# Kernel optimization log

Measured on AMD Instinct MI355X. Metric: run time of the kernel, lower is better.

The kernel has to match this reference:

```python
import jax, jax.numpy as jnp
import numpy as np

N, F, H, O = 16384, 64, 128, 512

def setup_inputs() -> dict:
    key = jax.random.key(0)
    ks = jax.random.split(key, 5)
    # PyTorch Linear default init: U(-1/sqrt(fan_in), 1/sqrt(fan_in))
    lim1 = 1.0  # fan_in = 1 for Linear(1, H)
    lim2 = 1.0 / np.sqrt(H)
    x = jax.random.normal(ks[0], (N, F), dtype=jnp.float32)
    W1 = jax.random.uniform(ks[1], (F, H), minval=-lim1, maxval=lim1, dtype=jnp.float32)
    b1 = jax.random.uniform(ks[2], (F, H), minval=-lim1, maxval=lim1, dtype=jnp.float32)
    W2 = jax.random.uniform(ks[3], (F, H, O), minval=-lim2, maxval=lim2, dtype=jnp.float32)
    b2 = jax.random.uniform(ks[4], (F, O), minval=-lim2, maxval=lim2, dtype=jnp.float32)
    return {"x": x, "W1": W1, "b1": b1, "W2": W2, "b2": b2}

def reference(x, W1, b1, W2, b2):
    # Per-feature MLP: h_f = W2_f @ elu(x_f * w1_f + b1_f) + b2_f, summed over f.
    # pre: [N, F, H] = outer-product of each scalar feature with its W1 row
    pre = x[:, :, None] * W1[None, :, :] + b1[None, :, :]
    a = jax.nn.elu(pre)                                  # [N, F, H]
    h = jnp.einsum('nfh,fho->no', a, W2)                 # sum over f and h
    h = h + jnp.sum(b2, axis=0)[None, :]                 # biases summed over F
    return h / jnp.sqrt(jnp.float32(F))
```

## Files before the change

### kernel.cpp

```cpp
#include <hip/hip_runtime.h>
#include <cstdint>

#define NROWS 16384
#define FDIM 64
#define HDIM 128
#define ODIM 512
#define KDIM 8192

#define BM 128
#define BN 256
#define BK 64
#define NSTEPS (KDIM / BK)

typedef short bf16x8 __attribute__((ext_vector_type(8)));
typedef float f32x4 __attribute__((ext_vector_type(4)));
typedef uint32_t u32x4 __attribute__((ext_vector_type(4)));

__device__ __forceinline__ uint16_t rne_bf16(float f) {
  uint32_t u = __builtin_bit_cast(uint32_t, f);
  u += 0x7fffu + ((u >> 16) & 1u);
  return (uint16_t)(u >> 16);
}

__global__ void prep_w2t(const float* __restrict__ W2, uint16_t* __restrict__ W2T) {
  __shared__ float tile[64][65];
  const int k0 = blockIdx.x * 64;
  const int o0 = blockIdx.y * 64;
  const int tx = threadIdx.x;
  const int ty = threadIdx.y;
#pragma unroll
  for (int j = 0; j < 8; ++j)
    tile[ty + 8 * j][tx] = W2[(size_t)(k0 + ty + 8 * j) * ODIM + o0 + tx];
  __syncthreads();
#pragma unroll
  for (int j = 0; j < 8; ++j)
    W2T[(size_t)(o0 + ty + 8 * j) * KDIM + k0 + tx] = rne_bf16(tile[tx][ty + 8 * j]);
}

__global__ void prep_b2sum(const float* __restrict__ b2, float* __restrict__ b2sum) {
  const int t = blockIdx.x * 256 + threadIdx.x;
  float s = 0.f;
#pragma unroll
  for (int f = 0; f < FDIM; ++f) s += b2[(size_t)f * ODIM + t];
  b2sum[t] = s;
}

__global__ __launch_bounds__(512, 2) void mlp_gemm(
    const float* __restrict__ x, const float* __restrict__ W1,
    const float* __restrict__ b1, const uint16_t* __restrict__ W2T,
    const float* __restrict__ b2sum, float* __restrict__ out) {
  __shared__ __align__(16) uint16_t As0[BM * BK];
  __shared__ __align__(16) uint16_t As1[BM * BK];
  __shared__ __align__(16) uint16_t Bs0[BN * BK];
  __shared__ __align__(16) uint16_t Bs1[BN * BK];

  const int tid = threadIdx.x;
  const int bid = blockIdx.x;
  const int g = bid & 7;
  const int o0 = (g >> 2) * BN;
  const int m0 = ((bid >> 3) * 4 + (g & 3)) * BM;

  const int wid = tid >> 6;
  const int lane = tid & 63;
  const int wm = wid >> 2;
  const int wni = wid & 3;
  const int q = lane >> 4;
  const int r = lane & 15;

  const int ar = tid >> 3;
  const int ac = tid & 7;
  const int brow = lane >> 3;
  const int bcg = (lane & 7) ^ brow;

  const float* xp0 = x + (size_t)(m0 + ar) * FDIM;
  const float* xp1 = x + (size_t)(m0 + 64 + ar) * FDIM;
  const int aw0 = ar * BK + ((ac ^ (ar & 7)) * 8);
  const int aw1 = (ar + 64) * BK + ((ac ^ (ar & 7)) * 8);

  f32x4 acc[4][4];
#pragma unroll
  for (int i = 0; i < 4; ++i)
#pragma unroll
    for (int j = 0; j < 4; ++j) acc[i][j] = {0.f, 0.f, 0.f, 0.f};

  auto stage = [&](uint16_t* Ab, uint16_t* Bb, int kk) {
#pragma unroll
    for (int j = 0; j < 4; ++j) {
      const int chunk = wid * 4 + j;
      const uint16_t* gp =
          W2T + (size_t)(o0 + chunk * 8 + brow) * KDIM + kk * BK + bcg * 8;
      uint16_t* lp = Bb + chunk * 512;
      __builtin_amdgcn_global_load_lds(
          (const __attribute__((address_space(1))) uint32_t*)gp,
          (__attribute__((address_space(3))) uint32_t*)lp, 16, 0, 0);
    }
    const int f = kk >> 1;
    const int hoff = (kk & 1) * 64 + ac * 8;
    const float xv0 = xp0[f];
    const float xv1 = xp1[f];
    float w1f[8], b1f[8];
    *(f32x4*)&w1f[0] = *(const f32x4*)(W1 + (size_t)f * HDIM + hoff);
    *(f32x4*)&w1f[4] = *(const f32x4*)(W1 + (size_t)f * HDIM + hoff + 4);
    *(f32x4*)&b1f[0] = *(const f32x4*)(b1 + (size_t)f * HDIM + hoff);
    *(f32x4*)&b1f[4] = *(const f32x4*)(b1 + (size_t)f * HDIM + hoff + 4);
    u32x4 ov0, ov1;
#pragma unroll
    for (int p = 0; p < 4; ++p) {
      float a0 = fmaf(xv0, w1f[2 * p], b1f[2 * p]);
      float a1 = fmaf(xv0, w1f[2 * p + 1], b1f[2 * p + 1]);
      float c0 = fmaf(xv1, w1f[2 * p], b1f[2 * p]);
      float c1 = fmaf(xv1, w1f[2 * p + 1], b1f[2 * p + 1]);
      float e0 = fmaxf(a0, __expf(fminf(a0, 0.f)) - 1.f);
      float e1 = fmaxf(a1, __expf(fminf(a1, 0.f)) - 1.f);
      float g0 = fmaxf(c0, __expf(fminf(c0, 0.f)) - 1.f);
      float g1 = fmaxf(c1, __expf(fminf(c1, 0.f)) - 1.f);
      ov0[p] = __builtin_amdgcn_perm(__builtin_bit_cast(uint32_t, e1),
                                     __builtin_bit_cast(uint32_t, e0), 0x07060302u);
      ov1[p] = __builtin_amdgcn_perm(__builtin_bit_cast(uint32_t, g1),
                                     __builtin_bit_cast(uint32_t, g0), 0x07060302u);
    }
    *(u32x4*)(Ab + aw0) = ov0;
    *(u32x4*)(Ab + aw1) = ov1;
  };

  auto compute = [&](const uint16_t* Ab, const uint16_t* Bb) {
#pragma unroll
    for (int kc = 0; kc < 2; ++kc) {
      const int cg = kc * 4 + q;
      bf16x8 af[4], bfr[4];
#pragma unroll
      for (int mt = 0; mt < 4; ++mt) {
        const int row = wm * 64 + mt * 16 + r;
        af[mt] = *(const bf16x8*)&Ab[row * BK + ((cg ^ (row & 7)) * 8)];
      }
#pragma unroll
      for (int nt = 0; nt < 4; ++nt) {
        const int row = wni * 64 + nt * 16 + r;
        bfr[nt] = *(const bf16x8*)&Bb[row * BK + ((cg ^ (row & 7)) * 8)];
      }
#pragma unroll
      for (int mt = 0; mt < 4; ++mt)
#pragma unroll
        for (int nt = 0; nt < 4; ++nt)
          acc[mt][nt] = __builtin_amdgcn_mfma_f32_16x16x32_bf16(
              af[mt], bfr[nt], acc[mt][nt], 0, 0, 0);
    }
  };

  stage(As0, Bs0, 0);
  __syncthreads();

#pragma unroll 1
  for (int kk = 0; kk < NSTEPS - 2; kk += 2) {
    stage(As1, Bs1, kk + 1);
    compute(As0, Bs0);
    __syncthreads();
    stage(As0, Bs0, kk + 2);
    compute(As1, Bs1);
    __syncthreads();
  }
  stage(As1, Bs1, NSTEPS - 1);
  compute(As0, Bs0);
  __syncthreads();
  compute(As1, Bs1);

  float bsv[4];
#pragma unroll
  for (int nt = 0; nt < 4; ++nt) bsv[nt] = b2sum[o0 + wni * 64 + nt * 16 + r];
#pragma unroll
  for (int mt = 0; mt < 4; ++mt)
#pragma unroll
    for (int nt = 0; nt < 4; ++nt)
#pragma unroll
      for (int v = 0; v < 4; ++v) {
        const int row = m0 + wm * 64 + mt * 16 + q * 4 + v;
        const int col = o0 + wni * 64 + nt * 16 + r;
        out[(size_t)row * ODIM + col] = (acc[mt][nt][v] + bsv[nt]) * 0.125f;
      }
}

extern "C" void kernel_launch(void* const* d_in, const int* in_sizes, int n_in,
                              void* d_out, int out_size, void* d_ws, size_t ws_size,
                              hipStream_t stream) {
  const float* x  = (const float*)d_in[0];
  const float* W1 = (const float*)d_in[1];
  const float* b1 = (const float*)d_in[2];
  const float* W2 = (const float*)d_in[3];
  const float* b2 = (const float*)d_in[4];
  float* out = (float*)d_out;

  char* ws = (char*)d_ws;
  float*    b2sum = (float*)ws;
  uint16_t* W2T   = (uint16_t*)(ws + 65536);

  prep_w2t<<<dim3(KDIM / 64, ODIM / 64), dim3(64, 8), 0, stream>>>(W2, W2T);
  prep_b2sum<<<2, 256, 0, stream>>>(b2, b2sum);
  mlp_gemm<<<256, 512, 0, stream>>>(x, W1, b1, W2T, b2sum, out);
}
```

Baseline: 271.1 us.

## Enlarge M tile to 256, split K in two, and prefetch W1/b1/x operands

```diff
diff --git a/kernel.cpp b/kernel.cpp
--- a/kernel.cpp
+++ b/kernel.cpp
@@ -7,10 +7,9 @@
 #define ODIM 512
 #define KDIM 8192
 
-#define BM 128
+#define BM 256
 #define BN 256
 #define BK 64
-#define NSTEPS (KDIM / BK)
 
 typedef short bf16x8 __attribute__((ext_vector_type(8)));
 typedef float f32x4 __attribute__((ext_vector_type(4)));
@@ -45,10 +44,27 @@
   b2sum[t] = s;
 }
 
+__global__ void combine_out(const float* __restrict__ p1, const float* __restrict__ b2sum,
+                            float* __restrict__ out) {
+  const size_t i = ((size_t)blockIdx.x * 256 + threadIdx.x) * 4;
+  f32x4 a = *(const f32x4*)(out + i);
+  f32x4 b = *(const f32x4*)(p1 + i);
+  f32x4 s = *(const f32x4*)(b2sum + (i & 511));
+  *(f32x4*)(out + i) = (a + b + s) * 0.125f;
+}
+
+struct RegSet {
+  f32x4 w1lo, w1hi, b1lo, b1hi;
+  float xv[4];
+};
+
+template <int KSPLIT>
 __global__ __launch_bounds__(512, 2) void mlp_gemm(
     const float* __restrict__ x, const float* __restrict__ W1,
     const float* __restrict__ b1, const uint16_t* __restrict__ W2T,
-    const float* __restrict__ b2sum, float* __restrict__ out) {
+    const float* __restrict__ b2sum, float* __restrict__ out,
+    float* __restrict__ part1) {
+  constexpr int NST = (KDIM / BK) / KSPLIT;
   __shared__ __align__(16) uint16_t As0[BM * BK];
   __shared__ __align__(16) uint16_t As1[BM * BK];
   __shared__ __align__(16) uint16_t Bs0[BN * BK];
@@ -56,9 +72,20 @@
 
   const int tid = threadIdx.x;
   const int bid = blockIdx.x;
-  const int g = bid & 7;
-  const int o0 = (g >> 2) * BN;
-  const int m0 = ((bid >> 3) * 4 + (g & 3)) * BM;
+
+  int o0, ko, m_idx;
+  if constexpr (KSPLIT == 2) {
+    const int g = bid & 7;
+    o0 = (g >> 2) * BN;
+    ko = g & 1;
+    m_idx = (bid >> 3) * 2 + ((g >> 1) & 1);
+  } else {
+    o0 = (bid & 1) * BN;
+    ko = 0;
+    m_idx = bid >> 1;
+  }
+  const int m0 = m_idx * BM;
+  const int kbase = ko * NST;
 
   const int wid = tid >> 6;
   const int lane = tid & 63;
@@ -69,68 +96,80 @@
 
   const int ar = tid >> 3;
   const int ac = tid & 7;
+  const int awc = (ac ^ (ar & 7)) * 8;
   const int brow = lane >> 3;
   const int bcg = (lane & 7) ^ brow;
 
-  const float* xp0 = x + (size_t)(m0 + ar) * FDIM;
-  const float* xp1 = x + (size_t)(m0 + 64 + ar) * FDIM;
-  const int aw0 = ar * BK + ((ac ^ (ar & 7)) * 8);
-  const int aw1 = (ar + 64) * BK + ((ac ^ (ar & 7)) * 8);
-
-  f32x4 acc[4][4];
-#pragma unroll
-  for (int i = 0; i < 4; ++i)
+  const float* xrow[4];
+#pragma unroll
+  for (int i = 0; i < 4; ++i) xrow[i] = x + (size_t)(m0 + i * 64 + ar) * FDIM;
+
+  f32x4 acc[8][4];
+#pragma unroll
+  for (int i = 0; i < 8; ++i)
 #pragma unroll
     for (int j = 0; j < 4; ++j) acc[i][j] = {0.f, 0.f, 0.f, 0.f};
 
-  auto stage = [&](uint16_t* Ab, uint16_t* Bb, int kk) {
+  auto preload = [&](RegSet& s, int kk) {
+    const int ks = kbase + kk;
+    const int fidx = ks >> 1;
+    const int ho = ((ks & 1) << 6) + ac * 8;
+    const float* wp = W1 + (size_t)fidx * HDIM + ho;
+    const float* bp = b1 + (size_t)fidx * HDIM + ho;
+    s.w1lo = *(const f32x4*)wp;
+    s.w1hi = *(const f32x4*)(wp + 4);
+    s.b1lo = *(const f32x4*)bp;
+    s.b1hi = *(const f32x4*)(bp + 4);
+#pragma unroll
+    for (int i = 0; i < 4; ++i) s.xv[i] = xrow[i][fidx];
+  };
+
+  auto stageB = [&](uint16_t* Bb, int kk) {
+    const int ks = kbase + kk;
 #pragma unroll
     for (int j = 0; j < 4; ++j) {
       const int chunk = wid * 4 + j;
       const uint16_t* gp =
-          W2T + (size_t)(o0 + chunk * 8 + brow) * KDIM + kk * BK + bcg * 8;
+          W2T + (size_t)(o0 + chunk * 8 + brow) * KDIM + ks * BK + bcg * 8;
       uint16_t* lp = Bb + chunk * 512;
       __builtin_amdgcn_global_load_lds(
           (const __attribute__((address_space(1))) uint32_t*)gp,
           (__attribute__((address_space(3))) uint32_t*)lp, 16, 0, 0);
     }
-    const int f = kk >> 1;
-    const int hoff = (kk & 1) * 64 + ac * 8;
-    const float xv0 = xp0[f];
-    const float xv1 = xp1[f];
-    float w1f[8], b1f[8];
-    *(f32x4*)&w1f[0] = *(const f32x4*)(W1 + (size_t)f * HDIM + hoff);
-    *(f32x4*)&w1f[4] = *(const f32x4*)(W1 + (size_t)f * HDIM + hoff + 4);
-    *(f32x4*)&b1f[0] = *(const f32x4*)(b1 + (size_t)f * HDIM + hoff);
-    *(f32x4*)&b1f[4] = *(const f32x4*)(b1 + (size_t)f * HDIM + hoff + 4);
-    u32x4 ov0, ov1;
+  };
+
+  auto elu_write = [&](uint16_t* Ab, const RegSet& s) {
+    float w[8], b[8];
 #pragma unroll
     for (int p = 0; p < 4; ++p) {
-      float a0 = fmaf(xv0, w1f[2 * p], b1f[2 * p]);
-      float a1 = fmaf(xv0, w1f[2 * p + 1], b1f[2 * p + 1]);
-      float c0 = fmaf(xv1, w1f[2 * p], b1f[2 * p]);
-      float c1 = fmaf(xv1, w1f[2 * p + 1], b1f[2 * p + 1]);
-      float e0 = fmaxf(a0, __expf(fminf(a0, 0.f)) - 1.f);
-      float e1 = fmaxf(a1, __expf(fminf(a1, 0.f)) - 1.f);
-      float g0 = fmaxf(c0, __expf(fminf(c0, 0.f)) - 1.f);
-      float g1 = fmaxf(c1, __expf(fminf(c1, 0.f)) - 1.f);
-      ov0[p] = __builtin_amdgcn_perm(__builtin_bit_cast(uint32_t, e1),
-                                     __builtin_bit_cast(uint32_t, e0), 0x07060302u);
-      ov1[p] = __builtin_amdgcn_perm(__builtin_bit_cast(uint32_t, g1),
-                                     __builtin_bit_cast(uint32_t, g0), 0x07060302u);
-    }
-    *(u32x4*)(Ab + aw0) = ov0;
-    *(u32x4*)(Ab + aw1) = ov1;
+      w[p] = s.w1lo[p]; w[p + 4] = s.w1hi[p];
+      b[p] = s.b1lo[p]; b[p + 4] = s.b1hi[p];
+    }
+#pragma unroll
+    for (int i = 0; i < 4; ++i) {
+      u32x4 ov;
+#pragma unroll
+      for (int p = 0; p < 4; ++p) {
+        float plo = fmaf(s.xv[i], w[2 * p], b[2 * p]);
+        float phi = fmaf(s.xv[i], w[2 * p + 1], b[2 * p + 1]);
+        float elo = fmaxf(plo, __expf(fminf(plo, 0.f)) - 1.f);
+        float ehi = fmaxf(phi, __expf(fminf(phi, 0.f)) - 1.f);
+        ov[p] = __builtin_amdgcn_perm(__builtin_bit_cast(uint32_t, ehi),
+                                      __builtin_bit_cast(uint32_t, elo),
+                                      0x07060302u);
+      }
+      *(u32x4*)(Ab + (i * 64 + ar) * BK + awc) = ov;
+    }
   };
 
   auto compute = [&](const uint16_t* Ab, const uint16_t* Bb) {
 #pragma unroll
     for (int kc = 0; kc < 2; ++kc) {
       const int cg = kc * 4 + q;
-      bf16x8 af[4], bfr[4];
-#pragma unroll
-      for (int mt = 0; mt < 4; ++mt) {
-        const int row = wm * 64 + mt * 16 + r;
+      bf16x8 af[8], bfr[4];
+#pragma unroll
+      for (int mt = 0; mt < 8; ++mt) {
+        const int row = wm * 128 + mt * 16 + r;
         af[mt] = *(const bf16x8*)&Ab[row * BK + ((cg ^ (row & 7)) * 8)];
       }
 #pragma unroll
@@ -139,7 +178,7 @@
         bfr[nt] = *(const bf16x8*)&Bb[row * BK + ((cg ^ (row & 7)) * 8)];
       }
 #pragma unroll
-      for (int mt = 0; mt < 4; ++mt)
+      for (int mt = 0; mt < 8; ++mt)
 #pragma unroll
         for (int nt = 0; nt < 4; ++nt)
           acc[mt][nt] = __builtin_amdgcn_mfma_f32_16x16x32_bf16(
@@ -147,36 +186,59 @@
     }
   };
 
-  stage(As0, Bs0, 0);
+  RegSet s0, s1;
+  preload(s0, 0);
+  stageB(Bs0, 0);
+  preload(s1, 1);
+  elu_write(As0, s0);
   __syncthreads();
 
 #pragma unroll 1
-  for (int kk = 0; kk < NSTEPS - 2; kk += 2) {
-    stage(As1, Bs1, kk + 1);
+  for (int kk = 0; kk < NST - 2; kk += 2) {
+    preload(s0, kk + 2);
+    stageB(Bs1, kk + 1);
+    elu_write(As1, s1);
     compute(As0, Bs0);
     __syncthreads();
-    stage(As0, Bs0, kk + 2);
+    preload(s1, kk + 3);
+    stageB(Bs0, kk + 2);
+    elu_write(As0, s0);
     compute(As1, Bs1);
     __syncthreads();
   }
-  stage(As1, Bs1, NSTEPS - 1);
+  stageB(Bs1, NST - 1);
+  elu_write(As1, s1);
   compute(As0, Bs0);
   __syncthreads();
   compute(As1, Bs1);
 
-  float bsv[4];
-#pragma unroll
-  for (int nt = 0; nt < 4; ++nt) bsv[nt] = b2sum[o0 + wni * 64 + nt * 16 + r];
-#pragma unroll
-  for (int mt = 0; mt < 4; ++mt)
-#pragma unroll
-    for (int nt = 0; nt < 4; ++nt)
-#pragma unroll
-      for (int v = 0; v < 4; ++v) {
-        const int row = m0 + wm * 64 + mt * 16 + q * 4 + v;
-        const int col = o0 + wni * 64 + nt * 16 + r;
-        out[(size_t)row * ODIM + col] = (acc[mt][nt][v] + bsv[nt]) * 0.125f;
-      }
+  if constexpr (KSPLIT == 2) {
+    float* P = ko ? part1 : out;
+#pragma unroll
+    for (int mt = 0; mt < 8; ++mt)
+#pragma unroll
+      for (int nt = 0; nt < 4; ++nt)
+#pragma unroll
+        for (int v = 0; v < 4; ++v) {
+          const int row = m0 + wm * 128 + mt * 16 + q * 4 + v;
+          const int col = o0 + wni * 64 + nt * 16 + r;
+          P[(size_t)row * ODIM + col] = acc[mt][nt][v];
+        }
+  } else {
+    float bsv[4];
+#pragma unroll
+    for (int nt = 0; nt < 4; ++nt) bsv[nt] = b2sum[o0 + wni * 64 + nt * 16 + r];
+#pragma unroll
+    for (int mt = 0; mt < 8; ++mt)
+#pragma unroll
+      for (int nt = 0; nt < 4; ++nt)
+#pragma unroll
+        for (int v = 0; v < 4; ++v) {
+          const int row = m0 + wm * 128 + mt * 16 + q * 4 + v;
+          const int col = o0 + wni * 64 + nt * 16 + r;
+          out[(size_t)row * ODIM + col] = (acc[mt][nt][v] + bsv[nt]) * 0.125f;
+        }
+  }
 }
 
 extern "C" void kernel_launch(void* const* d_in, const int* in_sizes, int n_in,
@@ -190,10 +252,20 @@
   float* out = (float*)d_out;
 
   char* ws = (char*)d_ws;
+  const size_t W2T_OFF = 65536;
+  const size_t P1_OFF = W2T_OFF + (size_t)ODIM * KDIM * 2;
+  const size_t NEED = P1_OFF + (size_t)NROWS * ODIM * 4;
   float*    b2sum = (float*)ws;
-  uint16_t* W2T   = (uint16_t*)(ws + 65536);
+  uint16_t* W2T   = (uint16_t*)(ws + W2T_OFF);
+  float*    part1 = (float*)(ws + P1_OFF);
 
   prep_w2t<<<dim3(KDIM / 64, ODIM / 64), dim3(64, 8), 0, stream>>>(W2, W2T);
   prep_b2sum<<<2, 256, 0, stream>>>(b2, b2sum);
-  mlp_gemm<<<256, 512, 0, stream>>>(x, W1, b1, W2T, b2sum, out);
-}
+
+  if (ws_size >= NEED) {
+    mlp_gemm<2><<<256, 512, 0, stream>>>(x, W1, b1, W2T, b2sum, out, part1);
+    combine_out<<<(NROWS * ODIM) / 1024, 256, 0, stream>>>(part1, b2sum, out);
+  } else {
+    mlp_gemm<1><<<128, 512, 0, stream>>>(x, W1, b1, W2T, b2sum, out, nullptr);
+  }
+}
```

New measurement: 299.8 us. 10.6% more time.
